# Optimization experiments

Measured on AMD Instinct MI355X. Metric: run time of the kernel, lower is better.

Reference implementation:

```python
import jax, jax.numpy as jnp
import numpy as np

BN_EPS = 1e-5


def setup_inputs() -> dict:
    key = jax.random.key(0)
    ks = jax.random.split(key, 13)
    B, C, H, W = 8, 256, 96, 32
    D = C // 2  # inter_channels
    s = 0.05
    return {
        "x": jax.random.normal(ks[0], (B, C, H, W), jnp.float32),
        "g_w": jax.random.normal(ks[1], (D, C), jnp.float32) * s,
        "g_b": jax.random.normal(ks[2], (D,), jnp.float32) * s,
        "theta_w": jax.random.normal(ks[3], (D, C), jnp.float32) * s,
        "theta_b": jax.random.normal(ks[4], (D,), jnp.float32) * s,
        "phi_w": jax.random.normal(ks[5], (D, C), jnp.float32) * s,
        "phi_b": jax.random.normal(ks[6], (D,), jnp.float32) * s,
        "w_w": jax.random.normal(ks[7], (C, D), jnp.float32) * s,
        "w_b": jax.random.normal(ks[8], (C,), jnp.float32) * s,
        "bn_gamma": jax.random.normal(ks[9], (C,), jnp.float32),
        "bn_beta": jax.random.normal(ks[10], (C,), jnp.float32) * s,
        "bn_mean": jax.random.normal(ks[11], (C,), jnp.float32) * s,
        "bn_var": jax.random.uniform(ks[12], (C,), jnp.float32),
    }


def reference(x, g_w, g_b, theta_w, theta_b, phi_w, phi_b, w_w, w_b,
              bn_gamma, bn_beta, bn_mean, bn_var):
    B, C, H, W = x.shape
    N = H * W
    xf = x.reshape(B, C, N)  # flatten spatial: (B, C, N)

    # 1x1 conv projections == per-pixel linear maps
    g_x = jnp.einsum('dc,bcn->bnd', g_w, xf) + g_b            # (B, N, D)
    theta_x = jnp.einsum('dc,bcn->bnd', theta_w, xf) + theta_b  # (B, N, D)
    phi_x = jnp.einsum('dc,bcn->bdn', phi_w, xf) + phi_b[:, None]  # (B, D, N)

    # unnormalized attention: f = theta phi^T / N, then y = f g
    f_div_C = jnp.einsum('bnd,bdm->bnm', theta_x, phi_x) / N  # (B, N, N)
    y = jnp.einsum('bnm,bmd->bnd', f_div_C, g_x)              # (B, N, D)

    # output 1x1 conv + eval-mode BatchNorm2d
    wy = jnp.einsum('cd,bnd->bcn', w_w, y) + w_b[:, None]     # (B, C, N)
    inv = bn_gamma / jnp.sqrt(bn_var + BN_EPS)
    wy = (wy - bn_mean[:, None]) * inv[:, None] + bn_beta[:, None]

    z = wy.reshape(B, C, H, W) + x  # residual
    return z
```

## Files before the change

### kernel.cpp

```cpp
#include <hip/hip_runtime.h>
#include <hip/hip_bf16.h>
#include <cstddef>

typedef __attribute__((ext_vector_type(8))) short short8;
typedef __attribute__((ext_vector_type(4))) float floatx4;
typedef __hip_bfloat16 bf16;

#define NB 8
#define NC 256
#define ND 128
#define NN 3072
#define NBLK 48
#define BN_EPS 1e-5f

static __device__ __forceinline__ short f2s(float v) {
    bf16 h = __float2bfloat16(v);
    return *reinterpret_cast<short*>(&h);
}

__global__ __launch_bounds__(256) void setup_kernel(
    const float* __restrict__ phi_w, const float* __restrict__ g_w,
    const float* __restrict__ theta_w, short* __restrict__ Wall)
{
    int t = threadIdx.x;
    int r = blockIdx.x;
    const float* src = (r < 128) ? (phi_w + (size_t)r * NC)
                     : (r < 256) ? (g_w + (size_t)(r - 128) * NC)
                                 : (theta_w + (size_t)(r - 256) * NC);
    Wall[(size_t)r * NC + t] = f2s(src[t]);
}

__global__ __launch_bounds__(384)
void proj_kernel(const float* __restrict__ x, const short* __restrict__ Wall,
                 const float* __restrict__ phi_b, const float* __restrict__ g_b,
                 const float* __restrict__ theta_b,
                 short* __restrict__ thDN, float* __restrict__ Mpart)
{
    __shared__ short PGs[256][72];
    __shared__ short Xs[64][72];
    int b = blockIdx.y;
    int n0 = blockIdx.x * 64;
    int t = threadIdx.x;
    int lane = t & 63;
    int wave = t >> 6;
    int lm = lane & 15;
    int lk = (lane >> 4) * 8;

    const float* xb = x + (size_t)b * NC * NN;

    floatx4 zero = {0.f, 0.f, 0.f, 0.f};
    floatx4 acc[4][4];
#pragma unroll
    for (int i = 0; i < 4; ++i)
#pragma unroll
        for (int j = 0; j < 4; ++j) acc[i][j] = zero;

#pragma unroll
    for (int kt = 0; kt < NC; kt += 64) {
        __syncthreads();
        if (t < 256) {
            int sn = t & 63, cg = t >> 6;
            const float* src = xb + (size_t)(kt + cg * 16) * NN + n0 + sn;
            short8 s0, s1;
#pragma unroll
            for (int j = 0; j < 8; ++j) {
                s0[j] = f2s(src[(size_t)j * NN]);
                s1[j] = f2s(src[(size_t)(8 + j) * NN]);
            }
            *(short8*)&Xs[sn][cg * 16]     = s0;
            *(short8*)&Xs[sn][cg * 16 + 8] = s1;
        }
        __syncthreads();
#pragma unroll
        for (int kk = 0; kk < 64; kk += 32) {
            short8 af[4], bfr[4];
#pragma unroll
            for (int i = 0; i < 4; ++i)
                af[i] = *(const short8*)(Wall +
                        (size_t)(wave * 64 + i * 16 + lm) * NC + kt + kk + lk);
#pragma unroll
            for (int j = 0; j < 4; ++j)
                bfr[j] = *(const short8*)&Xs[j * 16 + lm][kk + lk];
#pragma unroll
            for (int i = 0; i < 4; ++i)
#pragma unroll
                for (int j = 0; j < 4; ++j)
                    acc[i][j] = __builtin_amdgcn_mfma_f32_16x16x32_bf16(
                        af[i], bfr[j], acc[i][j], 0, 0, 0);
        }
    }

    int row0 = wave * 64 + (lane >> 4) * 4;

    if (wave < 4) {
#pragma unroll
        for (int i = 0; i < 4; ++i) {
#pragma unroll
            for (int r = 0; r < 4; ++r) {
                int row = row0 + i * 16 + r;
                float bv = (row < 128) ? phi_b[row] : g_b[row - 128];
#pragma unroll
                for (int j = 0; j < 4; ++j)
                    PGs[row][lm + j * 16] = f2s(acc[i][j][r] + bv);
            }
        }
    } else {
        short* Tb = thDN + (size_t)b * ND * NN;
#pragma unroll
        for (int i = 0; i < 4; ++i) {
#pragma unroll
            for (int r = 0; r < 4; ++r) {
                int d = row0 - 256 + i * 16 + r;
                float bv = theta_b[d];
#pragma unroll
                for (int j = 0; j < 4; ++j)
                    Tb[(size_t)d * NN + n0 + lm + j * 16] =
                        f2s(acc[i][j][r] + bv);
            }
        }
    }
    __syncthreads();

    if (wave < 4) {
        int wr = wave >> 1, wc = wave & 1;
        floatx4 macc[4][4];
#pragma unroll
        for (int i = 0; i < 4; ++i)
#pragma unroll
            for (int j = 0; j < 4; ++j) macc[i][j] = zero;
#pragma unroll
        for (int kk = 0; kk < 64; kk += 32) {
            short8 af[4], bfr[4];
#pragma unroll
            for (int i = 0; i < 4; ++i)
                af[i] = *(const short8*)&PGs[wr * 64 + i * 16 + lm][kk + lk];
#pragma unroll
            for (int j = 0; j < 4; ++j)
                bfr[j] = *(const short8*)&PGs[128 + wc * 64 + j * 16 + lm][kk + lk];
#pragma unroll
            for (int i = 0; i < 4; ++i)
#pragma unroll
                for (int j = 0; j < 4; ++j)
                    macc[i][j] = __builtin_amdgcn_mfma_f32_16x16x32_bf16(
                        af[i], bfr[j], macc[i][j], 0, 0, 0);
        }
        float* Mf = Mpart + ((size_t)b * NBLK + blockIdx.x) * (ND * ND);
        int mr0 = wr * 64 + (lane >> 4) * 4;
        int mc0 = wc * 64 + lm;
        const float sc = 1.f / (float)NN;
#pragma unroll
        for (int i = 0; i < 4; ++i)
#pragma unroll
            for (int j = 0; j < 4; ++j)
#pragma unroll
                for (int r = 0; r < 4; ++r)
                    Mf[(size_t)(mr0 + i * 16 + r) * ND + mc0 + j * 16] =
                        macc[i][j][r] * sc;
    }
}

__global__ __launch_bounds__(256)
void reduce_kernel(const float* __restrict__ Mpart, short* __restrict__ Mb16)
{
    int idx = blockIdx.x * 256 + threadIdx.x;
    int b = idx >> 14;
    int e = idx & 16383;
    const float* src = Mpart + (size_t)b * NBLK * 16384 + e;
    float s = 0.f;
#pragma unroll 8
    for (int p = 0; p < NBLK; ++p) s += src[(size_t)p * 16384];
    Mb16[(size_t)b * 16384 + e] = f2s(s);
}

__global__ __launch_bounds__(256)
void final_kernel(const short* __restrict__ Mb16, const short* __restrict__ thDN,
                  const float* __restrict__ w_w, const float* __restrict__ w_b,
                  const float* __restrict__ gamma, const float* __restrict__ beta,
                  const float* __restrict__ mean, const float* __restrict__ var,
                  const float* __restrict__ x, float* __restrict__ out)
{
    __shared__ short As[128][72];
    __shared__ short Bs[128][72];
    __shared__ short P2s[128][136];
    int b = blockIdx.z;
    int tile_m = blockIdx.y * 128;
    int tile_n = blockIdx.x * 128;
    int t = threadIdx.x;
    int lane = t & 63;
    int wave = t >> 6;
    int wr = wave >> 1, wc = wave & 1;
    int lm = lane & 15;
    int lk = (lane >> 4) * 8;
    int ch = (t & 7) * 8;
    int r0 = t >> 3;

    const short* Mb = Mb16 + (size_t)b * ND * ND;

    floatx4 zero = {0.f, 0.f, 0.f, 0.f};
    floatx4 acc[4][4];
#pragma unroll
    for (int i = 0; i < 4; ++i)
#pragma unroll
        for (int j = 0; j < 4; ++j) acc[i][j] = zero;

#pragma unroll
    for (int kt = 0; kt < ND; kt += 64) {
        __syncthreads();
#pragma unroll
        for (int p = 0; p < 4; ++p) {
            int r = r0 + p * 32;
            const float* ap = w_w + (size_t)(tile_m + r) * ND + kt + ch;
            floatx4 a0 = *(const floatx4*)ap, a1 = *(const floatx4*)(ap + 4);
            short8 sa;
#pragma unroll
            for (int j = 0; j < 4; ++j) { sa[j] = f2s(a0[j]); sa[4 + j] = f2s(a1[j]); }
            *(short8*)&As[r][ch] = sa;
            *(short8*)&Bs[r][ch] = *(const short8*)(Mb + (size_t)r * ND + kt + ch);
        }
        __syncthreads();
#pragma unroll
        for (int kk = 0; kk < 64; kk += 32) {
            short8 af[4], bfr[4];
#pragma unroll
            for (int i = 0; i < 4; ++i)
                af[i] = *(const short8*)&As[wr * 64 + i * 16 + lm][kk + lk];
#pragma unroll
            for (int j = 0; j < 4; ++j)
                bfr[j] = *(const short8*)&Bs[wc * 64 + j * 16 + lm][kk + lk];
#pragma unroll
            for (int i = 0; i < 4; ++i)
#pragma unroll
                for (int j = 0; j < 4; ++j)
                    acc[i][j] = __builtin_amdgcn_mfma_f32_16x16x32_bf16(
                        af[i], bfr[j], acc[i][j], 0, 0, 0);
        }
    }

    {
        int row0 = wr * 64 + (lane >> 4) * 4;
        int col0 = wc * 64 + lm;
#pragma unroll
        for (int i = 0; i < 4; ++i) {
#pragma unroll
            for (int r = 0; r < 4; ++r) {
                int cl = row0 + i * 16 + r;
                int c = tile_m + cl;
                float iv = gamma[c] * rsqrtf(var[c] + BN_EPS);
#pragma unroll
                for (int j = 0; j < 4; ++j)
                    P2s[cl][col0 + j * 16] = f2s(acc[i][j][r] * iv);
            }
        }
    }

    floatx4 acc2[4][4];
#pragma unroll
    for (int i = 0; i < 4; ++i)
#pragma unroll
        for (int j = 0; j < 4; ++j) acc2[i][j] = zero;

    const short* Tb = thDN + (size_t)b * ND * NN;
#pragma unroll
    for (int kt = 0; kt < ND; kt += 64) {
        __syncthreads();
        {
            int dl = t & 63;
            int ng = t >> 6;
            const short* src = Tb + (size_t)(kt + dl) * NN + tile_n + ng * 32;
#pragma unroll
            for (int q = 0; q < 4; ++q) {
                short8 v = *(const short8*)(src + q * 8);
#pragma unroll
                for (int jj = 0; jj < 8; ++jj)
                    Bs[ng * 32 + q * 8 + jj][dl] = v[jj];
            }
        }
        __syncthreads();
#pragma unroll
        for (int kk = 0; kk < 64; kk += 32) {
            short8 af[4], bfr[4];
#pragma unroll
            for (int i = 0; i < 4; ++i)
                af[i] = *(const short8*)&P2s[wr * 64 + i * 16 + lm][kt + kk + lk];
#pragma unroll
            for (int j = 0; j < 4; ++j)
                bfr[j] = *(const short8*)&Bs[wc * 64 + j * 16 + lm][kk + lk];
#pragma unroll
            for (int i = 0; i < 4; ++i)
#pragma unroll
                for (int j = 0; j < 4; ++j)
                    acc2[i][j] = __builtin_amdgcn_mfma_f32_16x16x32_bf16(
                        af[i], bfr[j], acc2[i][j], 0, 0, 0);
        }
    }

    int crow0 = tile_m + wr * 64 + (lane >> 4) * 4;
    int col0 = tile_n + wc * 64 + lm;
    float* Cf = out + (size_t)b * NC * NN;
    const float* Rg = x + (size_t)b * NC * NN;
#pragma unroll
    for (int i = 0; i < 4; ++i) {
#pragma unroll
        for (int r = 0; r < 4; ++r) {
            int c = crow0 + i * 16 + r;
            float iv = gamma[c] * rsqrtf(var[c] + BN_EPS);
            float b2 = iv * (w_b[c] - mean[c]) + beta[c];
#pragma unroll
            for (int j = 0; j < 4; ++j) {
                size_t idx = (size_t)c * NN + col0 + j * 16;
                Cf[idx] = acc2[i][j][r] + b2 + Rg[idx];
            }
        }
    }
}

extern "C" void kernel_launch(void* const* d_in, const int* in_sizes, int n_in,
                              void* d_out, int out_size, void* d_ws, size_t ws_size,
                              hipStream_t stream)
{
    const float* x       = (const float*)d_in[0];
    const float* g_w     = (const float*)d_in[1];
    const float* g_b     = (const float*)d_in[2];
    const float* theta_w = (const float*)d_in[3];
    const float* theta_b = (const float*)d_in[4];
    const float* phi_w   = (const float*)d_in[5];
    const float* phi_b   = (const float*)d_in[6];
    const float* w_w     = (const float*)d_in[7];
    const float* w_b     = (const float*)d_in[8];
    const float* gamma   = (const float*)d_in[9];
    const float* beta    = (const float*)d_in[10];
    const float* mean    = (const float*)d_in[11];
    const float* var     = (const float*)d_in[12];
    (void)in_sizes; (void)n_in; (void)out_size; (void)ws_size;

    char* w = (char*)d_ws;
    short* thDN  = (short*)w; w += (size_t)NB * ND * NN * 2;
    float* Mpart = (float*)w; w += (size_t)NB * NBLK * ND * ND * 4;
    short* Mb16  = (short*)w; w += (size_t)NB * ND * ND * 2;
    short* Wall  = (short*)w; w += (size_t)384 * NC * 2;

    setup_kernel<<<dim3(384), dim3(256), 0, stream>>>(
        phi_w, g_w, theta_w, Wall);

    proj_kernel<<<dim3(NN / 64, NB), dim3(384), 0, stream>>>(
        x, Wall, phi_b, g_b, theta_b, thDN, Mpart);

    reduce_kernel<<<dim3(512), dim3(256), 0, stream>>>(Mpart, Mb16);

    final_kernel<<<dim3(NN / 128, NC / 128, NB), 256, 0, stream>>>(
        Mb16, thDN, w_w, w_b, gamma, beta, mean, var, x, (float*)d_out);
}
```

Before: 137.8 us.

## Register-prefetch next tiles in proj and final kernels, vectorize reduce

In the projection kernel, the next 64-channel slab of x is loaded into registers while the current slab is used for MFMA work, and the weight fragments are loaded before the LDS barrier. The final kernel preloads the w_w/M tiles and the theta tiles for the second GEMM into registers ahead of each barrier, so global-load latency overlaps with compute. The reduce kernel now uses float4 loads with a quarter of the blocks. The trade-off is higher register pressure, which may reduce occupancy.

Result: faster. 133.6 us (-3.1%).

```diff
diff --git a/kernel.cpp b/kernel.cpp
--- a/kernel.cpp
+++ b/kernel.cpp
@@ -3,6 +3,7 @@
 #include <cstddef>
 
 typedef __attribute__((ext_vector_type(8))) short short8;
+typedef __attribute__((ext_vector_type(4))) short short4v;
 typedef __attribute__((ext_vector_type(4))) float floatx4;
 typedef __hip_bfloat16 bf16;
 
@@ -55,29 +56,44 @@
 #pragma unroll
         for (int j = 0; j < 4; ++j) acc[i][j] = zero;
 
+    int sn = t & 63, cg = t >> 6;
+    const float* srcp = xb + (size_t)(cg * 16) * NN + n0 + sn;
+    float xf[16];
+    if (t < 256) {
+#pragma unroll
+        for (int j = 0; j < 16; ++j) xf[j] = srcp[(size_t)j * NN];
+    }
+
 #pragma unroll
     for (int kt = 0; kt < NC; kt += 64) {
         __syncthreads();
+        short8 af2[2][4];
+#pragma unroll
+        for (int h = 0; h < 2; ++h)
+#pragma unroll
+            for (int i = 0; i < 4; ++i)
+                af2[h][i] = *(const short8*)(Wall +
+                        (size_t)(wave * 64 + i * 16 + lm) * NC + kt + h * 32 + lk);
         if (t < 256) {
-            int sn = t & 63, cg = t >> 6;
-            const float* src = xb + (size_t)(kt + cg * 16) * NN + n0 + sn;
             short8 s0, s1;
 #pragma unroll
             for (int j = 0; j < 8; ++j) {
-                s0[j] = f2s(src[(size_t)j * NN]);
-                s1[j] = f2s(src[(size_t)(8 + j) * NN]);
+                s0[j] = f2s(xf[j]);
+                s1[j] = f2s(xf[8 + j]);
             }
             *(short8*)&Xs[sn][cg * 16]     = s0;
             *(short8*)&Xs[sn][cg * 16 + 8] = s1;
         }
         __syncthreads();
-#pragma unroll
-        for (int kk = 0; kk < 64; kk += 32) {
-            short8 af[4], bfr[4];
-#pragma unroll
-            for (int i = 0; i < 4; ++i)
-                af[i] = *(const short8*)(Wall +
-                        (size_t)(wave * 64 + i * 16 + lm) * NC + kt + kk + lk);
+        if (t < 256 && kt < NC - 64) {
+            const float* np = srcp + (size_t)(kt + 64) * NN;
+#pragma unroll
+            for (int j = 0; j < 16; ++j) xf[j] = np[(size_t)j * NN];
+        }
+#pragma unroll
+        for (int h = 0; h < 2; ++h) {
+            int kk = h * 32;
+            short8 bfr[4];
 #pragma unroll
             for (int j = 0; j < 4; ++j)
                 bfr[j] = *(const short8*)&Xs[j * 16 + lm][kk + lk];
@@ -86,7 +102,7 @@
 #pragma unroll
                 for (int j = 0; j < 4; ++j)
                     acc[i][j] = __builtin_amdgcn_mfma_f32_16x16x32_bf16(
-                        af[i], bfr[j], acc[i][j], 0, 0, 0);
+                        af2[h][i], bfr[j], acc[i][j], 0, 0, 0);
         }
     }
 
@@ -162,14 +178,17 @@
 __global__ __launch_bounds__(256)
 void reduce_kernel(const float* __restrict__ Mpart, short* __restrict__ Mb16)
 {
-    int idx = blockIdx.x * 256 + threadIdx.x;
-    int b = idx >> 14;
-    int e = idx & 16383;
-    const float* src = Mpart + (size_t)b * NBLK * 16384 + e;
-    float s = 0.f;
-#pragma unroll 8
-    for (int p = 0; p < NBLK; ++p) s += src[(size_t)p * 16384];
-    Mb16[(size_t)b * 16384 + e] = f2s(s);
+    int idx4 = (blockIdx.x * 256 + threadIdx.x) * 4;
+    const float* src = Mpart + (size_t)(idx4 >> 14) * (NBLK * 16384)
+                             + (idx4 & 16383);
+    floatx4 s = {0.f, 0.f, 0.f, 0.f};
+#pragma unroll 12
+    for (int p = 0; p < NBLK; ++p)
+        s += *(const floatx4*)(src + (size_t)p * 16384);
+    short4v o;
+#pragma unroll
+    for (int j = 0; j < 4; ++j) o[j] = f2s(s[j]);
+    *(short4v*)(Mb16 + idx4) = o;
 }
 
 __global__ __launch_bounds__(256)
@@ -193,8 +212,12 @@
     int lk = (lane >> 4) * 8;
     int ch = (t & 7) * 8;
     int r0 = t >> 3;
+    int dl = t & 63;
+    int ng = t >> 6;
 
     const short* Mb = Mb16 + (size_t)b * ND * ND;
+    const short* Tb = thDN + (size_t)b * ND * NN;
+    const short* tsrc = Tb + (size_t)dl * NN + tile_n + ng * 32;
 
     floatx4 zero = {0.f, 0.f, 0.f, 0.f};
     floatx4 acc[4][4];
@@ -203,21 +226,48 @@
 #pragma unroll
         for (int j = 0; j < 4; ++j) acc[i][j] = zero;
 
+    floatx4 av0[4], av1[4];
+    short8 bv[4];
+#pragma unroll
+    for (int p = 0; p < 4; ++p) {
+        int r = r0 + p * 32;
+        const float* ap = w_w + (size_t)(tile_m + r) * ND + ch;
+        av0[p] = *(const floatx4*)ap;
+        av1[p] = *(const floatx4*)(ap + 4);
+        bv[p]  = *(const short8*)(Mb + (size_t)r * ND + ch);
+    }
+    short8 tv[4];
+
 #pragma unroll
     for (int kt = 0; kt < ND; kt += 64) {
         __syncthreads();
 #pragma unroll
         for (int p = 0; p < 4; ++p) {
             int r = r0 + p * 32;
-            const float* ap = w_w + (size_t)(tile_m + r) * ND + kt + ch;
-            floatx4 a0 = *(const floatx4*)ap, a1 = *(const floatx4*)(ap + 4);
             short8 sa;
 #pragma unroll
-            for (int j = 0; j < 4; ++j) { sa[j] = f2s(a0[j]); sa[4 + j] = f2s(a1[j]); }
+            for (int j = 0; j < 4; ++j) {
+                sa[j]     = f2s(av0[p][j]);
+                sa[4 + j] = f2s(av1[p][j]);
+            }
             *(short8*)&As[r][ch] = sa;
-            *(short8*)&Bs[r][ch] = *(const short8*)(Mb + (size_t)r * ND + kt + ch);
-        }
-        __syncthreads();
+            *(short8*)&Bs[r][ch] = bv[p];
+        }
+        __syncthreads();
+        if (kt == 0) {
+#pragma unroll
+            for (int p = 0; p < 4; ++p) {
+                int r = r0 + p * 32;
+                const float* ap = w_w + (size_t)(tile_m + r) * ND + 64 + ch;
+                av0[p] = *(const floatx4*)ap;
+                av1[p] = *(const floatx4*)(ap + 4);
+                bv[p]  = *(const short8*)(Mb + (size_t)r * ND + 64 + ch);
+            }
+        } else {
+#pragma unroll
+            for (int q = 0; q < 4; ++q)
+                tv[q] = *(const short8*)(tsrc + q * 8);
+        }
 #pragma unroll
         for (int kk = 0; kk < 64; kk += 32) {
             short8 af[4], bfr[4];
@@ -259,23 +309,20 @@
 #pragma unroll
         for (int j = 0; j < 4; ++j) acc2[i][j] = zero;
 
-    const short* Tb = thDN + (size_t)b * ND * NN;
 #pragma unroll
     for (int kt = 0; kt < ND; kt += 64) {
         __syncthreads();
-        {
-            int dl = t & 63;
-            int ng = t >> 6;
-            const short* src = Tb + (size_t)(kt + dl) * NN + tile_n + ng * 32;
-#pragma unroll
-            for (int q = 0; q < 4; ++q) {
-                short8 v = *(const short8*)(src + q * 8);
-#pragma unroll
-                for (int jj = 0; jj < 8; ++jj)
-                    Bs[ng * 32 + q * 8 + jj][dl] = v[jj];
-            }
-        }
-        __syncthreads();
+#pragma unroll
+        for (int q = 0; q < 4; ++q)
+#pragma unroll
+            for (int jj = 0; jj < 8; ++jj)
+                Bs[ng * 32 + q * 8 + jj][dl] = tv[q][jj];
+        __syncthreads();
+        if (kt == 0) {
+#pragma unroll
+            for (int q = 0; q < 4; ++q)
+                tv[q] = *(const short8*)(tsrc + (size_t)64 * NN + q * 8);
+        }
 #pragma unroll
         for (int kk = 0; kk < 64; kk += 32) {
             short8 af[4], bfr[4];
@@ -345,7 +392,7 @@
     proj_kernel<<<dim3(NN / 64, NB), dim3(384), 0, stream>>>(
         x, Wall, phi_b, g_b, theta_b, thDN, Mpart);
 
-    reduce_kernel<<<dim3(512), dim3(256), 0, stream>>>(Mpart, Mb16);
+    reduce_kernel<<<dim3(128), dim3(256), 0, stream>>>(Mpart, Mb16);
 
     final_kernel<<<dim3(NN / 128, NC / 128, NB), 256, 0, stream>>>(
         Mb16, thDN, w_w, w_b, gamma, beta, mean, var, x, (float*)d_out);
```

## Reassociate attention via per-batch Gram matrix and fold weights into single output GEMM

Applied to the files above, without the earlier changes.

The non-local block is re-associated algebraically. The code computes the Gram matrix X·Xᵀ per batch with split-K partials and a reduce, then chains small GEMMs in one block per batch (phi_w·G·g_wᵀ plus bias terms from channel sums, then w_w, then theta_w) into a combined 256x256 matrix Q and a per-channel constant. A final kernel applies Q to x with the residual added. This drops the separate theta projection and its store and load, but the chain_kernel runs on only 8 blocks, and the bf16 rounding of intermediate products changes numerics.

Result: slower. 236.4 us (+71.5%).

```diff
diff --git a/kernel.cpp b/kernel.cpp
--- a/kernel.cpp
+++ b/kernel.cpp
@@ -3,6 +3,7 @@
 #include <cstddef>
 
 typedef __attribute__((ext_vector_type(8))) short short8;
+typedef __attribute__((ext_vector_type(4))) short short4v;
 typedef __attribute__((ext_vector_type(4))) float floatx4;
 typedef __hip_bfloat16 bf16;
 
@@ -10,7 +11,7 @@
 #define NC 256
 #define ND 128
 #define NN 3072
-#define NBLK 48
+#define NKC 16
 #define BN_EPS 1e-5f
 
 static __device__ __forceinline__ short f2s(float v) {
@@ -18,35 +19,59 @@
     return *reinterpret_cast<short*>(&h);
 }
 
-__global__ __launch_bounds__(256) void setup_kernel(
-    const float* __restrict__ phi_w, const float* __restrict__ g_w,
-    const float* __restrict__ theta_w, short* __restrict__ Wall)
-{
+static __device__ __forceinline__ short8 ld8cvt(const float* p) {
+    floatx4 a = *(const floatx4*)p, b = *(const floatx4*)(p + 4);
+    short8 r;
+    r[0] = f2s(a[0]); r[1] = f2s(a[1]); r[2] = f2s(a[2]); r[3] = f2s(a[3]);
+    r[4] = f2s(b[0]); r[5] = f2s(b[1]); r[6] = f2s(b[2]); r[7] = f2s(b[3]);
+    return r;
+}
+
+__global__ __launch_bounds__(256)
+void pre_kernel(const float* __restrict__ x, const float* __restrict__ theta_w,
+                float* __restrict__ sx, short* __restrict__ thwT)
+{
+    int blk = blockIdx.x;
     int t = threadIdx.x;
-    int r = blockIdx.x;
-    const float* src = (r < 128) ? (phi_w + (size_t)r * NC)
-                     : (r < 256) ? (g_w + (size_t)(r - 128) * NC)
-                                 : (theta_w + (size_t)(r - 256) * NC);
-    Wall[(size_t)r * NC + t] = f2s(src[t]);
-}
-
-__global__ __launch_bounds__(384)
-void proj_kernel(const float* __restrict__ x, const short* __restrict__ Wall,
-                 const float* __restrict__ phi_b, const float* __restrict__ g_b,
-                 const float* __restrict__ theta_b,
-                 short* __restrict__ thDN, float* __restrict__ Mpart)
-{
-    __shared__ short PGs[256][72];
-    __shared__ short Xs[64][72];
-    int b = blockIdx.y;
-    int n0 = blockIdx.x * 64;
-    int t = threadIdx.x;
-    int lane = t & 63;
-    int wave = t >> 6;
-    int lm = lane & 15;
-    int lk = (lane >> 4) * 8;
-
+    if (blk < 256) {
+        int b = blk >> 5;
+        int c0 = (blk & 31) * 8;
+        int r = t >> 5;
+        int w32 = t & 31;
+        const float* xr = x + ((size_t)b * NC + c0 + r) * NN;
+        float s = 0.f;
+#pragma unroll
+        for (int k = 0; k < 24; ++k) {
+            floatx4 v = *(const floatx4*)(xr + (size_t)(w32 + k * 32) * 4);
+            s += v[0] + v[1] + v[2] + v[3];
+        }
+#pragma unroll
+        for (int off = 16; off; off >>= 1) s += __shfl_down(s, off, 32);
+        if (w32 == 0) sx[b * NC + c0 + r] = s;
+    } else {
+        int c0 = (blk - 256) * 32;
+        int cl = t >> 3;
+        int e0 = (t & 7) * 16;
+#pragma unroll
+        for (int j = 0; j < 16; ++j)
+            thwT[(size_t)(c0 + cl) * ND + e0 + j] =
+                f2s(theta_w[(size_t)(e0 + j) * NC + c0 + cl]);
+    }
+}
+
+__global__ __launch_bounds__(256)
+void gpart_kernel(const float* __restrict__ x, float* __restrict__ Gpart)
+{
+    int blk = blockIdx.x;
+    int tile = blk & 3;
+    int kc = (blk >> 2) & 15;
+    int b = blk >> 6;
+    int tr = tile >> 1, tc = tile & 1;
+    int t = threadIdx.x, lane = t & 63, wave = t >> 6;
+    int wr = wave >> 1, wc = wave & 1;
+    int lm = lane & 15, lh = lane >> 4, lk = lh * 8;
     const float* xb = x + (size_t)b * NC * NN;
+    int n0 = kc * (NN / NKC);
 
     floatx4 zero = {0.f, 0.f, 0.f, 0.f};
     floatx4 acc[4][4];
@@ -56,259 +81,327 @@
         for (int j = 0; j < 4; ++j) acc[i][j] = zero;
 
 #pragma unroll
-    for (int kt = 0; kt < NC; kt += 64) {
-        __syncthreads();
-        if (t < 256) {
-            int sn = t & 63, cg = t >> 6;
-            const float* src = xb + (size_t)(kt + cg * 16) * NN + n0 + sn;
-            short8 s0, s1;
-#pragma unroll
-            for (int j = 0; j < 8; ++j) {
-                s0[j] = f2s(src[(size_t)j * NN]);
-                s1[j] = f2s(src[(size_t)(8 + j) * NN]);
-            }
-            *(short8*)&Xs[sn][cg * 16]     = s0;
-            *(short8*)&Xs[sn][cg * 16 + 8] = s1;
-        }
-        __syncthreads();
-#pragma unroll
-        for (int kk = 0; kk < 64; kk += 32) {
-            short8 af[4], bfr[4];
-#pragma unroll
-            for (int i = 0; i < 4; ++i)
-                af[i] = *(const short8*)(Wall +
-                        (size_t)(wave * 64 + i * 16 + lm) * NC + kt + kk + lk);
+    for (int kk = 0; kk < 192; kk += 32) {
+        short8 af[4], bf[4];
+#pragma unroll
+        for (int i = 0; i < 4; ++i)
+            af[i] = ld8cvt(xb + (size_t)(tr * 128 + wr * 64 + i * 16 + lm) * NN
+                           + n0 + kk + lk);
+#pragma unroll
+        for (int j = 0; j < 4; ++j)
+            bf[j] = ld8cvt(xb + (size_t)(tc * 128 + wc * 64 + j * 16 + lm) * NN
+                           + n0 + kk + lk);
+#pragma unroll
+        for (int i = 0; i < 4; ++i)
 #pragma unroll
             for (int j = 0; j < 4; ++j)
-                bfr[j] = *(const short8*)&Xs[j * 16 + lm][kk + lk];
-#pragma unroll
-            for (int i = 0; i < 4; ++i)
-#pragma unroll
-                for (int j = 0; j < 4; ++j)
-                    acc[i][j] = __builtin_amdgcn_mfma_f32_16x16x32_bf16(
-                        af[i], bfr[j], acc[i][j], 0, 0, 0);
-        }
-    }
-
-    int row0 = wave * 64 + (lane >> 4) * 4;
-
-    if (wave < 4) {
-#pragma unroll
-        for (int i = 0; i < 4; ++i) {
-#pragma unroll
-            for (int r = 0; r < 4; ++r) {
-                int row = row0 + i * 16 + r;
-                float bv = (row < 128) ? phi_b[row] : g_b[row - 128];
-#pragma unroll
-                for (int j = 0; j < 4; ++j)
-                    PGs[row][lm + j * 16] = f2s(acc[i][j][r] + bv);
-            }
-        }
-    } else {
-        short* Tb = thDN + (size_t)b * ND * NN;
-#pragma unroll
-        for (int i = 0; i < 4; ++i) {
-#pragma unroll
-            for (int r = 0; r < 4; ++r) {
-                int d = row0 - 256 + i * 16 + r;
-                float bv = theta_b[d];
-#pragma unroll
-                for (int j = 0; j < 4; ++j)
-                    Tb[(size_t)d * NN + n0 + lm + j * 16] =
-                        f2s(acc[i][j][r] + bv);
-            }
-        }
-    }
-    __syncthreads();
-
-    if (wave < 4) {
-        int wr = wave >> 1, wc = wave & 1;
-        floatx4 macc[4][4];
-#pragma unroll
-        for (int i = 0; i < 4; ++i)
-#pragma unroll
-            for (int j = 0; j < 4; ++j) macc[i][j] = zero;
-#pragma unroll
-        for (int kk = 0; kk < 64; kk += 32) {
-            short8 af[4], bfr[4];
-#pragma unroll
-            for (int i = 0; i < 4; ++i)
-                af[i] = *(const short8*)&PGs[wr * 64 + i * 16 + lm][kk + lk];
-#pragma unroll
-            for (int j = 0; j < 4; ++j)
-                bfr[j] = *(const short8*)&PGs[128 + wc * 64 + j * 16 + lm][kk + lk];
-#pragma unroll
-            for (int i = 0; i < 4; ++i)
-#pragma unroll
-                for (int j = 0; j < 4; ++j)
-                    macc[i][j] = __builtin_amdgcn_mfma_f32_16x16x32_bf16(
-                        af[i], bfr[j], macc[i][j], 0, 0, 0);
-        }
-        float* Mf = Mpart + ((size_t)b * NBLK + blockIdx.x) * (ND * ND);
-        int mr0 = wr * 64 + (lane >> 4) * 4;
-        int mc0 = wc * 64 + lm;
-        const float sc = 1.f / (float)NN;
-#pragma unroll
-        for (int i = 0; i < 4; ++i)
-#pragma unroll
-            for (int j = 0; j < 4; ++j)
-#pragma unroll
-                for (int r = 0; r < 4; ++r)
-                    Mf[(size_t)(mr0 + i * 16 + r) * ND + mc0 + j * 16] =
-                        macc[i][j][r] * sc;
-    }
+                acc[i][j] = __builtin_amdgcn_mfma_f32_16x16x32_bf16(
+                    af[i], bf[j], acc[i][j], 0, 0, 0);
+    }
+    float* Gf = Gpart + (size_t)blk * 16384;
+#pragma unroll
+    for (int i = 0; i < 4; ++i)
+#pragma unroll
+        for (int j = 0; j < 4; ++j)
+#pragma unroll
+            for (int rr = 0; rr < 4; ++rr)
+                Gf[(size_t)(wr * 64 + i * 16 + lh * 4 + rr) * 128
+                   + wc * 64 + j * 16 + lm] = acc[i][j][rr];
 }
 
 __global__ __launch_bounds__(256)
-void reduce_kernel(const float* __restrict__ Mpart, short* __restrict__ Mb16)
+void gred_kernel(const float* __restrict__ Gpart, float* __restrict__ G)
 {
     int idx = blockIdx.x * 256 + threadIdx.x;
     int b = idx >> 14;
-    int e = idx & 16383;
-    const float* src = Mpart + (size_t)b * NBLK * 16384 + e;
-    float s = 0.f;
-#pragma unroll 8
-    for (int p = 0; p < NBLK; ++p) s += src[(size_t)p * 16384];
-    Mb16[(size_t)b * 16384 + e] = f2s(s);
+    int fo = (idx & 16383) * 4;
+    int c = fo >> 8;
+    int cp = fo & 255;
+    const float* src = Gpart + ((size_t)b * 64 + (size_t)((c >> 7) * 2 + (cp >> 7))) * 16384
+                     + (size_t)(c & 127) * 128 + (cp & 127);
+    floatx4 s = {0.f, 0.f, 0.f, 0.f};
+#pragma unroll
+    for (int k = 0; k < NKC; ++k)
+        s += *(const floatx4*)(src + (size_t)k * 65536);
+    *(floatx4*)(G + (size_t)b * 65536 + fo) = s;
 }
 
 __global__ __launch_bounds__(256)
-void final_kernel(const short* __restrict__ Mb16, const short* __restrict__ thDN,
+void chain_kernel(const float* __restrict__ G,
+                  const float* __restrict__ phi_w, const float* __restrict__ phi_b,
+                  const float* __restrict__ g_w, const float* __restrict__ g_b,
+                  const float* __restrict__ theta_b,
                   const float* __restrict__ w_w, const float* __restrict__ w_b,
                   const float* __restrict__ gamma, const float* __restrict__ beta,
                   const float* __restrict__ mean, const float* __restrict__ var,
-                  const float* __restrict__ x, float* __restrict__ out)
-{
-    __shared__ short As[128][72];
-    __shared__ short Bs[128][72];
-    __shared__ short P2s[128][136];
-    int b = blockIdx.z;
-    int tile_m = blockIdx.y * 128;
-    int tile_n = blockIdx.x * 128;
-    int t = threadIdx.x;
-    int lane = t & 63;
-    int wave = t >> 6;
+                  const float* __restrict__ sx, const short* __restrict__ thwT,
+                  float* __restrict__ T1g, float* __restrict__ Sg,
+                  float* __restrict__ W2g, short* __restrict__ QfB,
+                  float* __restrict__ C2g)
+{
+    __shared__ float sxl[256];
+    __shared__ float psxs[128], gsxs[128];
+    int b = blockIdx.x;
+    int t = threadIdx.x, lane = t & 63, wave = t >> 6;
+    int lm = lane & 15, lh = lane >> 4, lk = lh * 8;
     int wr = wave >> 1, wc = wave & 1;
-    int lm = lane & 15;
-    int lk = (lane >> 4) * 8;
-    int ch = (t & 7) * 8;
-    int r0 = t >> 3;
-
-    const short* Mb = Mb16 + (size_t)b * ND * ND;
-
+    const float* Gb = G + (size_t)b * 65536;
     floatx4 zero = {0.f, 0.f, 0.f, 0.f};
-    floatx4 acc[4][4];
-#pragma unroll
-    for (int i = 0; i < 4; ++i)
-#pragma unroll
-        for (int j = 0; j < 4; ++j) acc[i][j] = zero;
-
-#pragma unroll
-    for (int kt = 0; kt < ND; kt += 64) {
-        __syncthreads();
-#pragma unroll
-        for (int p = 0; p < 4; ++p) {
-            int r = r0 + p * 32;
-            const float* ap = w_w + (size_t)(tile_m + r) * ND + kt + ch;
-            floatx4 a0 = *(const floatx4*)ap, a1 = *(const floatx4*)(ap + 4);
-            short8 sa;
-#pragma unroll
-            for (int j = 0; j < 4; ++j) { sa[j] = f2s(a0[j]); sa[4 + j] = f2s(a1[j]); }
-            *(short8*)&As[r][ch] = sa;
-            *(short8*)&Bs[r][ch] = *(const short8*)(Mb + (size_t)r * ND + kt + ch);
-        }
-        __syncthreads();
-#pragma unroll
-        for (int kk = 0; kk < 64; kk += 32) {
-            short8 af[4], bfr[4];
-#pragma unroll
-            for (int i = 0; i < 4; ++i)
-                af[i] = *(const short8*)&As[wr * 64 + i * 16 + lm][kk + lk];
+
+    if (t < 64) *(floatx4*)&sxl[t * 4] = *(const floatx4*)(sx + b * NC + t * 4);
+    __syncthreads();
+    {
+        const float* wrow = (t < 128) ? (phi_w + (size_t)t * NC)
+                                      : (g_w + (size_t)(t - 128) * NC);
+        float s = 0.f;
+#pragma unroll
+        for (int k = 0; k < 64; ++k) {
+            floatx4 v = *(const floatx4*)(wrow + k * 4);
+            s += v[0]*sxl[k*4] + v[1]*sxl[k*4+1] + v[2]*sxl[k*4+2] + v[3]*sxl[k*4+3];
+        }
+        if (t < 128) psxs[t] = s; else gsxs[t - 128] = s;
+    }
+
+    {
+        floatx4 acc[4][8];
+#pragma unroll
+        for (int i = 0; i < 4; ++i)
+#pragma unroll
+            for (int j = 0; j < 8; ++j) acc[i][j] = zero;
+#pragma unroll
+        for (int kk = 0; kk < 256; kk += 32) {
+            short8 af[4], bf[8];
+#pragma unroll
+            for (int i = 0; i < 4; ++i)
+                af[i] = ld8cvt(phi_w + (size_t)(wr * 64 + i * 16 + lm) * NC + kk + lk);
+#pragma unroll
+            for (int j = 0; j < 8; ++j)
+                bf[j] = ld8cvt(Gb + (size_t)(wc * 128 + j * 16 + lm) * NC + kk + lk);
+#pragma unroll
+            for (int i = 0; i < 4; ++i)
+#pragma unroll
+                for (int j = 0; j < 8; ++j)
+                    acc[i][j] = __builtin_amdgcn_mfma_f32_16x16x32_bf16(
+                        af[i], bf[j], acc[i][j], 0, 0, 0);
+        }
+        float* T1b = T1g + (size_t)b * 32768;
+#pragma unroll
+        for (int i = 0; i < 4; ++i)
+#pragma unroll
+            for (int j = 0; j < 8; ++j)
+#pragma unroll
+                for (int rr = 0; rr < 4; ++rr)
+                    T1b[(size_t)(wr * 64 + i * 16 + lh * 4 + rr) * 256
+                        + wc * 128 + j * 16 + lm] = acc[i][j][rr];
+    }
+    __syncthreads();
+
+    {
+        const float* T1b = T1g + (size_t)b * 32768;
+        floatx4 acc[4][4];
+#pragma unroll
+        for (int i = 0; i < 4; ++i)
+#pragma unroll
+            for (int j = 0; j < 4; ++j) acc[i][j] = zero;
+#pragma unroll
+        for (int kk = 0; kk < 256; kk += 32) {
+            short8 af[4], bf[4];
+#pragma unroll
+            for (int i = 0; i < 4; ++i)
+                af[i] = ld8cvt(T1b + (size_t)(wr * 64 + i * 16 + lm) * 256 + kk + lk);
 #pragma unroll
             for (int j = 0; j < 4; ++j)
-                bfr[j] = *(const short8*)&Bs[wc * 64 + j * 16 + lm][kk + lk];
+                bf[j] = ld8cvt(g_w + (size_t)(wc * 64 + j * 16 + lm) * NC + kk + lk);
 #pragma unroll
             for (int i = 0; i < 4; ++i)
 #pragma unroll
                 for (int j = 0; j < 4; ++j)
                     acc[i][j] = __builtin_amdgcn_mfma_f32_16x16x32_bf16(
-                        af[i], bfr[j], acc[i][j], 0, 0, 0);
-        }
-    }
+                        af[i], bf[j], acc[i][j], 0, 0, 0);
+        }
+        float* Sb = Sg + (size_t)b * 16384;
+#pragma unroll
+        for (int i = 0; i < 4; ++i)
+#pragma unroll
+            for (int j = 0; j < 4; ++j)
+#pragma unroll
+                for (int rr = 0; rr < 4; ++rr) {
+                    int e = wr * 64 + i * 16 + lh * 4 + rr;
+                    int d = wc * 64 + j * 16 + lm;
+                    float v = acc[i][j][rr] + psxs[e] * g_b[d]
+                            + phi_b[e] * gsxs[d]
+                            + (float)NN * phi_b[e] * g_b[d];
+                    Sb[(size_t)e * 128 + d] = v;
+                }
+    }
+    __syncthreads();
 
     {
-        int row0 = wr * 64 + (lane >> 4) * 4;
-        int col0 = wc * 64 + lm;
-#pragma unroll
-        for (int i = 0; i < 4; ++i) {
-#pragma unroll
-            for (int r = 0; r < 4; ++r) {
-                int cl = row0 + i * 16 + r;
-                int c = tile_m + cl;
-                float iv = gamma[c] * rsqrtf(var[c] + BN_EPS);
-#pragma unroll
-                for (int j = 0; j < 4; ++j)
-                    P2s[cl][col0 + j * 16] = f2s(acc[i][j][r] * iv);
+        const float* Sb = Sg + (size_t)b * 16384;
+        floatx4 acc[4][8];
+#pragma unroll
+        for (int i = 0; i < 4; ++i)
+#pragma unroll
+            for (int j = 0; j < 8; ++j) acc[i][j] = zero;
+#pragma unroll
+        for (int kk = 0; kk < 128; kk += 32) {
+            short8 af[4], bf[8];
+#pragma unroll
+            for (int i = 0; i < 4; ++i)
+                af[i] = ld8cvt(w_w + (size_t)(wave * 64 + i * 16 + lm) * ND + kk + lk);
+#pragma unroll
+            for (int j = 0; j < 8; ++j)
+                bf[j] = ld8cvt(Sb + (size_t)(j * 16 + lm) * 128 + kk + lk);
+#pragma unroll
+            for (int i = 0; i < 4; ++i)
+#pragma unroll
+                for (int j = 0; j < 8; ++j)
+                    acc[i][j] = __builtin_amdgcn_mfma_f32_16x16x32_bf16(
+                        af[i], bf[j], acc[i][j], 0, 0, 0);
+        }
+        float* W2b = W2g + (size_t)b * 32768;
+#pragma unroll
+        for (int i = 0; i < 4; ++i)
+#pragma unroll
+            for (int j = 0; j < 8; ++j)
+#pragma unroll
+                for (int rr = 0; rr < 4; ++rr)
+                    W2b[(size_t)(wave * 64 + i * 16 + lh * 4 + rr) * 128
+                        + j * 16 + lm] = acc[i][j][rr];
+    }
+    __syncthreads();
+
+    {
+        const float* W2b = W2g + (size_t)b * 32768;
+#pragma unroll
+        for (int half = 0; half < 2; ++half) {
+            floatx4 acc[4][8];
+#pragma unroll
+            for (int i = 0; i < 4; ++i)
+#pragma unroll
+                for (int j = 0; j < 8; ++j) acc[i][j] = zero;
+#pragma unroll
+            for (int kk = 0; kk < 128; kk += 32) {
+                short8 af[4], bf[8];
+#pragma unroll
+                for (int i = 0; i < 4; ++i)
+                    af[i] = ld8cvt(W2b + (size_t)(wave * 64 + i * 16 + lm) * 128 + kk + lk);
+#pragma unroll
+                for (int j = 0; j < 8; ++j)
+                    bf[j] = *(const short8*)(thwT
+                            + (size_t)(half * 128 + j * 16 + lm) * ND + kk + lk);
+#pragma unroll
+                for (int i = 0; i < 4; ++i)
+#pragma unroll
+                    for (int j = 0; j < 8; ++j)
+                        acc[i][j] = __builtin_amdgcn_mfma_f32_16x16x32_bf16(
+                            af[i], bf[j], acc[i][j], 0, 0, 0);
             }
-        }
-    }
-
-    floatx4 acc2[4][4];
+#pragma unroll
+            for (int i = 0; i < 4; ++i)
+#pragma unroll
+                for (int rr = 0; rr < 4; ++rr) {
+                    int c = wave * 64 + i * 16 + lh * 4 + rr;
+                    float iv = gamma[c] * rsqrtf(var[c] + BN_EPS) * (1.f / (float)NN);
+#pragma unroll
+                    for (int j = 0; j < 8; ++j)
+                        QfB[(size_t)b * 65536 + (size_t)c * 256
+                            + half * 128 + j * 16 + lm] = f2s(acc[i][j][rr] * iv);
+                }
+        }
+        {
+            int c = t;
+            const float* wrow = W2b + (size_t)c * 128;
+            float s = 0.f;
+#pragma unroll
+            for (int e = 0; e < 128; ++e) s += wrow[e] * theta_b[e];
+            float iv = gamma[c] * rsqrtf(var[c] + BN_EPS);
+            C2g[b * NC + c] = iv * (s * (1.f / (float)NN) + w_b[c] - mean[c]) + beta[c];
+        }
+    }
+}
+
+__global__ __launch_bounds__(512, 2)
+void out_kernel(const short* __restrict__ QfB, const float* __restrict__ C2g,
+                const float* __restrict__ x, float* __restrict__ out)
+{
+    __shared__ short Xs[96][72];
+    int blk = blockIdx.x;
+    int b = blk >> 5;
+    int n0 = (blk & 31) * 96;
+    int t = threadIdx.x, lane = t & 63, wave = t >> 6;
+    int lm = lane & 15, lh = lane >> 4, lk = lh * 8;
+    int wr = wave >> 1, wc = wave & 1;
+    const float* xb = x + (size_t)b * NC * NN;
+    const short* Qb = QfB + (size_t)b * 65536;
+
+    floatx4 zero = {0.f, 0.f, 0.f, 0.f};
+    floatx4 acc[4][3];
 #pragma unroll
     for (int i = 0; i < 4; ++i)
 #pragma unroll
-        for (int j = 0; j < 4; ++j) acc2[i][j] = zero;
-
-    const short* Tb = thDN + (size_t)b * ND * NN;
-#pragma unroll
-    for (int kt = 0; kt < ND; kt += 64) {
+        for (int j = 0; j < 3; ++j) acc[i][j] = zero;
+
+    int sn = t % 96, cgp = t / 96;
+    float xf[16];
+    if (t < 384) {
+#pragma unroll
+        for (int j = 0; j < 16; ++j)
+            xf[j] = xb[(size_t)(cgp * 16 + j) * NN + n0 + sn];
+    }
+
+#pragma unroll
+    for (int kt = 0; kt < NC; kt += 64) {
         __syncthreads();
-        {
-            int dl = t & 63;
-            int ng = t >> 6;
-            const short* src = Tb + (size_t)(kt + dl) * NN + tile_n + ng * 32;
-#pragma unroll
-            for (int q = 0; q < 4; ++q) {
-                short8 v = *(const short8*)(src + q * 8);
-#pragma unroll
-                for (int jj = 0; jj < 8; ++jj)
-                    Bs[ng * 32 + q * 8 + jj][dl] = v[jj];
+        short8 af2[2][4];
+#pragma unroll
+        for (int h = 0; h < 2; ++h)
+#pragma unroll
+            for (int i = 0; i < 4; ++i)
+                af2[h][i] = *(const short8*)(Qb
+                        + (size_t)(wr * 64 + i * 16 + lm) * 256 + kt + h * 32 + lk);
+        if (t < 384) {
+            short8 s0, s1;
+#pragma unroll
+            for (int j = 0; j < 8; ++j) {
+                s0[j] = f2s(xf[j]);
+                s1[j] = f2s(xf[8 + j]);
             }
+            *(short8*)&Xs[sn][cgp * 16]     = s0;
+            *(short8*)&Xs[sn][cgp * 16 + 8] = s1;
         }
         __syncthreads();
-#pragma unroll
-        for (int kk = 0; kk < 64; kk += 32) {
-            short8 af[4], bfr[4];
-#pragma unroll
-            for (int i = 0; i < 4; ++i)
-                af[i] = *(const short8*)&P2s[wr * 64 + i * 16 + lm][kt + kk + lk];
-#pragma unroll
-            for (int j = 0; j < 4; ++j)
-                bfr[j] = *(const short8*)&Bs[wc * 64 + j * 16 + lm][kk + lk];
-#pragma unroll
-            for (int i = 0; i < 4; ++i)
-#pragma unroll
-                for (int j = 0; j < 4; ++j)
-                    acc2[i][j] = __builtin_amdgcn_mfma_f32_16x16x32_bf16(
-                        af[i], bfr[j], acc2[i][j], 0, 0, 0);
-        }
-    }
-
-    int crow0 = tile_m + wr * 64 + (lane >> 4) * 4;
-    int col0 = tile_n + wc * 64 + lm;
+        if (t < 384 && kt < NC - 64) {
+#pragma unroll
+            for (int j = 0; j < 16; ++j)
+                xf[j] = xb[(size_t)(kt + 64 + cgp * 16 + j) * NN + n0 + sn];
+        }
+#pragma unroll
+        for (int h = 0; h < 2; ++h) {
+            short8 bfr[3];
+#pragma unroll
+            for (int j = 0; j < 3; ++j)
+                bfr[j] = *(const short8*)&Xs[wc * 48 + j * 16 + lm][h * 32 + lk];
+#pragma unroll
+            for (int i = 0; i < 4; ++i)
+#pragma unroll
+                for (int j = 0; j < 3; ++j)
+                    acc[i][j] = __builtin_amdgcn_mfma_f32_16x16x32_bf16(
+                        af2[h][i], bfr[j], acc[i][j], 0, 0, 0);
+        }
+    }
+
     float* Cf = out + (size_t)b * NC * NN;
-    const float* Rg = x + (size_t)b * NC * NN;
 #pragma unroll
     for (int i = 0; i < 4; ++i) {
 #pragma unroll
-        for (int r = 0; r < 4; ++r) {
-            int c = crow0 + i * 16 + r;
-            float iv = gamma[c] * rsqrtf(var[c] + BN_EPS);
-            float b2 = iv * (w_b[c] - mean[c]) + beta[c];
-#pragma unroll
-            for (int j = 0; j < 4; ++j) {
-                size_t idx = (size_t)c * NN + col0 + j * 16;
-                Cf[idx] = acc2[i][j][r] + b2 + Rg[idx];
+        for (int rr = 0; rr < 4; ++rr) {
+            int c = wr * 64 + i * 16 + lh * 4 + rr;
+            float c2 = C2g[b * NC + c];
+#pragma unroll
+            for (int j = 0; j < 3; ++j) {
+                size_t idx = (size_t)c * NN + n0 + wc * 48 + j * 16 + lm;
+                Cf[idx] = acc[i][j][rr] + c2 + xb[idx];
             }
         }
     }
@@ -334,19 +427,25 @@
     (void)in_sizes; (void)n_in; (void)out_size; (void)ws_size;
 
     char* w = (char*)d_ws;
-    short* thDN  = (short*)w; w += (size_t)NB * ND * NN * 2;
-    float* Mpart = (float*)w; w += (size_t)NB * NBLK * ND * ND * 4;
-    short* Mb16  = (short*)w; w += (size_t)NB * ND * ND * 2;
-    short* Wall  = (short*)w; w += (size_t)384 * NC * 2;
-
-    setup_kernel<<<dim3(384), dim3(256), 0, stream>>>(
-        phi_w, g_w, theta_w, Wall);
-
-    proj_kernel<<<dim3(NN / 64, NB), dim3(384), 0, stream>>>(
-        x, Wall, phi_b, g_b, theta_b, thDN, Mpart);
-
-    reduce_kernel<<<dim3(512), dim3(256), 0, stream>>>(Mpart, Mb16);
-
-    final_kernel<<<dim3(NN / 128, NC / 128, NB), 256, 0, stream>>>(
-        Mb16, thDN, w_w, w_b, gamma, beta, mean, var, x, (float*)d_out);
-}
+    float* sx    = (float*)w; w += (size_t)NB * NC * 4;
+    float* C2g   = (float*)w; w += (size_t)NB * NC * 4;
+    short* thwT  = (short*)w; w += (size_t)NC * ND * 2;
+    float* Gpart = (float*)w; w += (size_t)NB * NKC * 4 * 16384 * 4;
+    float* G     = (float*)w; w += (size_t)NB * NC * NC * 4;
+    float* T1g   = (float*)w; w += (size_t)NB * ND * NC * 4;
+    float* Sg    = (float*)w; w += (size_t)NB * ND * ND * 4;
+    float* W2g   = (float*)w; w += (size_t)NB * NC * ND * 4;
+    short* QfB   = (short*)w; w += (size_t)NB * NC * NC * 2;
+
+    pre_kernel<<<dim3(264), dim3(256), 0, stream>>>(x, theta_w, sx, thwT);
+
+    gpart_kernel<<<dim3(NB * NKC * 4), dim3(256), 0, stream>>>(x, Gpart);
+
+    gred_kernel<<<dim3(512), dim3(256), 0, stream>>>(Gpart, G);
+
+    chain_kernel<<<dim3(NB), dim3(256), 0, stream>>>(
+        G, phi_w, phi_b, g_w, g_b, theta_b, w_w, w_b,
+        gamma, beta, mean, var, sx, thwT, T1g, Sg, W2g, QfB, C2g);
+
+    out_kernel<<<dim3(256), dim3(512), 0, stream>>>(QfB, C2g, x, (float*)d_out);
+}
```
